# Kernel tuning notes

Measured on AMD Instinct MI355X. Metric: run time of the kernel, lower is better.

The kernel has to match this reference:

```python
import jax, jax.numpy as jnp
import numpy as np

D = 4096       # hidden_size
H = 32         # n_heads (tp_size=1)
DN = 128       # qk_nope_head_dim
DR = 64        # qk_rope_head_dim
DV = 128       # v_head_dim
QL = 1536      # q_lora_rank
KL = 512       # kv_lora_rank
S = 2048       # seqlen, start_pos = 0
EPS = 1e-6
SCALE = (DN + DR) ** -0.5  # softmax_scale (no yarn mscale: seqlen <= original_seq_len)
THETA = 10000.0


def _freqs(seqlen, dim, base=THETA):
    # precompute_freqs_cis without yarn correction (seqlen <= original_seq_len)
    inv = 1.0 / (base ** (np.arange(0, dim, 2, dtype=np.float32) / dim))
    f = np.outer(np.arange(seqlen, dtype=np.float32), inv)  # [S, dim//2]
    return jnp.asarray(np.cos(f)), jnp.asarray(np.sin(f))


def _rmsnorm(x, w):
    return x * jax.lax.rsqrt(jnp.mean(x * x, axis=-1, keepdims=True) + EPS) * w


def _rope(x, cos, sin):
    # x: [S, H, R]; complex rotation on consecutive pairs (view_as_complex semantics)
    S_, H_, R_ = x.shape
    xr = x.reshape(S_, H_, R_ // 2, 2)
    x0, x1 = xr[..., 0], xr[..., 1]
    c = cos[:, None, :]
    s = sin[:, None, :]
    y0 = x0 * c - x1 * s
    y1 = x0 * s + x1 * c
    return jnp.stack([y0, y1], axis=-1).reshape(S_, H_, R_)


def setup_inputs() -> dict:
    key = jax.random.key(0)
    ks = jax.random.split(key, 6)
    std = 0.02
    return {
        "x": jax.random.normal(ks[0], (S, D), jnp.float32),
        "wq_a": jax.random.normal(ks[1], (QL, D), jnp.float32) * std,
        "q_norm_w": jnp.ones((QL,), jnp.float32),
        "wq_b": jax.random.normal(ks[2], (H * (DN + DR), QL), jnp.float32) * std,
        "wkv_a": jax.random.normal(ks[3], (KL + DR, D), jnp.float32) * std,
        "kv_norm_w": jnp.ones((KL,), jnp.float32),
        "wkv_b": jax.random.normal(ks[4], (H * (DN + DV), KL), jnp.float32) * std,
        "wo": jax.random.normal(ks[5], (D, H * DV), jnp.float32) * std,
    }


def reference(x, wq_a, q_norm_w, wq_b, wkv_a, kv_norm_w, wkv_b, wo):
    cos, sin = _freqs(S, DR)

    # q path: low-rank down-proj + RMSNorm + up-proj
    q = _rmsnorm(x @ wq_a.T, q_norm_w) @ wq_b.T          # [S, H*(DN+DR)]
    q = q.reshape(S, H, DN + DR)
    q_nope, q_pe = q[..., :DN], q[..., DN:]
    q_pe = _rope(q_pe, cos, sin)                          # [S, H, DR]

    # kv path: joint latent + rope part
    kv_all = x @ wkv_a.T                                  # [S, KL+DR]
    kv = _rmsnorm(kv_all[:, :KL], kv_norm_w)              # latent kv cache [S, KL]
    k_pe = _rope(kv_all[:, None, KL:], cos, sin)[:, 0, :]  # pe cache [S, DR]

    # absorb k-up-projection into q (einsum 'shd,hdc->shc')
    wkv_b_r = wkv_b.reshape(H, DN + DV, KL)
    q_lat = jnp.einsum("shd,hdc->shc", q_nope, wkv_b_r[:, :DN])  # [S, H, KL]

    scores = (jnp.einsum("shc,tc->sht", q_lat, kv)
              + jnp.einsum("shr,tr->sht", q_pe, k_pe)) * SCALE   # [S, H, T]

    causal = jnp.arange(S)[:, None] >= jnp.arange(S)[None, :]     # [S, T]
    scores = jnp.where(causal[:, None, :], scores, -jnp.inf)
    p = jax.nn.softmax(scores, axis=-1)

    o_lat = jnp.einsum("sht,tc->shc", p, kv)                      # [S, H, KL]
    o = jnp.einsum("shc,hdc->shd", o_lat, wkv_b_r[:, DN:])        # [S, H, DV]
    return o.reshape(S, H * DV) @ wo.T                            # [S, D]
```

## Files before the change

kernel.cpp:

```cpp
#include <hip/hip_runtime.h>
#include <hip/hip_bf16.h>
#include <type_traits>

using bf16 = __hip_bfloat16;
typedef short v8s __attribute__((ext_vector_type(8)));
typedef float v4f __attribute__((ext_vector_type(4)));

#define DEV __device__ __forceinline__

constexpr float SCALE_ = 0.07216878364870322f;

DEV unsigned short bfu(float f) {
  bf16 h = __float2bfloat16(f);
  return __builtin_bit_cast(unsigned short, h);
}
DEV float b2f(short u) {
  unsigned int x = ((unsigned int)(unsigned short)u) << 16;
  return __builtin_bit_cast(float, x);
}

DEV void g2lds16(const void* g, void* l) {
  __builtin_amdgcn_global_load_lds(
      (const __attribute__((address_space(1))) unsigned int*)g,
      (__attribute__((address_space(3))) unsigned int*)l, 16, 0, 0);
}


__global__ void cast_kernel(const float* __restrict__ in, bf16* __restrict__ out, int n4) {
  int i = blockIdx.x * 256 + threadIdx.x;
  int stride = gridDim.x * 256;
  for (; i < n4; i += stride) {
    float4 v = ((const float4*)in)[i];
    ushort4 u;
    u.x = bfu(v.x); u.y = bfu(v.y); u.z = bfu(v.z); u.w = bfu(v.w);
    ((ushort4*)out)[i] = u;
  }
}

__global__ void cast_pad_kernel(const float* __restrict__ in, bf16* __restrict__ out) {
  int i = blockIdx.x * 256 + threadIdx.x;
  float4 v = make_float4(0.f, 0.f, 0.f, 0.f);
  if (i < 589824) v = ((const float4*)in)[i];
  ushort4 u;
  u.x = bfu(v.x); u.y = bfu(v.y); u.z = bfu(v.z); u.w = bfu(v.w);
  ((ushort4*)out)[i] = u;
}

__global__ void wkvbt_kernel(const float* __restrict__ wkvb, bf16* __restrict__ out) {
  int gid = blockIdx.x * 256 + threadIdx.x;
  int c8 = (gid & 63) * 8;
  int d8 = ((gid >> 6) & 15) * 8;
  int h = gid >> 10;
  float4 a[8][2];
#pragma unroll
  for (int r = 0; r < 8; ++r) {
    const float* p = wkvb + ((long)(h * 256 + d8 + r)) * 512 + c8;
    a[r][0] = *(const float4*)p;
    a[r][1] = *(const float4*)(p + 4);
  }
#pragma unroll
  for (int cc = 0; cc < 8; ++cc) {
    v8s o;
#pragma unroll
    for (int r = 0; r < 8; ++r) {
      float f = (cc < 4) ? ((const float*)&a[r][0])[cc] : ((const float*)&a[r][1])[cc - 4];
      o[r] = (short)bfu(f);
    }
    *(v8s*)(out + (long)h * 65536 + (c8 + cc) * 128 + d8) = o;
  }
}

__global__ void wkvbv_kernel(const float* __restrict__ wkvb, bf16* __restrict__ out) {
  int i = blockIdx.x * 256 + threadIdx.x;
  int c4 = i & 127, d = (i >> 7) & 127, h = i >> 14;
  float4 v = *(const float4*)(wkvb + ((long)(h * 256 + 128 + d)) * 512 + c4 * 4);
  ushort4 u;
  u.x = bfu(v.x); u.y = bfu(v.y); u.z = bfu(v.z); u.w = bfu(v.w);
  *(ushort4*)(out + ((long)(h * 128 + d)) * 512 + c4 * 4) = u;
}

__global__ void freqs_kernel(float* __restrict__ cosb, float* __restrict__ sinb) {
  int t = blockIdx.x * 256 + threadIdx.x;
  int s = t >> 5, i = t & 31;
  float inv = powf(10000.0f, -(float)(2 * i) / 64.0f);
  float f = (float)s * inv;
  cosb[t] = cosf(f);
  sinb[t] = sinf(f);
}

__global__ void rmsnorm_bf_kernel(const bf16* __restrict__ in, const float* __restrict__ w,
                                  bf16* __restrict__ out, int L, int ldin, int ldout) {
  int row = blockIdx.x;
  const bf16* x = in + (long)row * ldin;
  int L8 = L >> 3;
  float ss = 0.f;
  for (int i = threadIdx.x; i < L8; i += 256) {
    v8s v = *(const v8s*)(x + i * 8);
#pragma unroll
    for (int j = 0; j < 8; ++j) { float f = b2f(v[j]); ss += f * f; }
  }
#pragma unroll
  for (int d = 1; d < 64; d <<= 1) ss += __shfl_xor(ss, d);
  __shared__ float red[4];
  if ((threadIdx.x & 63) == 0) red[threadIdx.x >> 6] = ss;
  __syncthreads();
  float r = rsqrtf((red[0] + red[1] + red[2] + red[3]) / (float)L + 1e-6f);
  bf16* o = out + (long)row * ldout;
  for (int i = threadIdx.x; i < L8; i += 256) {
    v8s v = *(const v8s*)(x + i * 8);
    v8s u;
#pragma unroll
    for (int j = 0; j < 8; ++j)
      u[j] = (short)bfu(b2f(v[j]) * r * w[i * 8 + j]);
    *(v8s*)(o + i * 8) = u;
  }
}

__global__ void rope_kpe_kernel(const bf16* __restrict__ kvall, const float* __restrict__ cosb,
                                const float* __restrict__ sinb, bf16* __restrict__ keff) {
  int t = blockIdx.x * 256 + threadIdx.x;
  int s = t >> 5, i = t & 31;
  const bf16* p = kvall + (long)s * 640 + 512;
  float x0 = __bfloat162float(p[2 * i]), x1 = __bfloat162float(p[2 * i + 1]);
  float c = cosb[t], sn = sinb[t];
  bf16* o = keff + (long)s * 576 + 512;
  o[2 * i] = __float2bfloat16(x0 * c - x1 * sn);
  o[2 * i + 1] = __float2bfloat16(x0 * sn + x1 * c);
}

__global__ void rope_q_kernel(const bf16* __restrict__ qf, const float* __restrict__ cosb,
                              const float* __restrict__ sinb, bf16* __restrict__ qeff) {
  int t = blockIdx.x * 256 + threadIdx.x;
  int i = t & 31, h = (t >> 5) & 31, s = t >> 10;
  const bf16* p = qf + (long)s * 6144 + h * 192 + 128;
  float x0 = __bfloat162float(p[2 * i]), x1 = __bfloat162float(p[2 * i + 1]);
  float c = cosb[s * 32 + i], sn = sinb[s * 32 + i];
  bf16* o = qeff + (long)s * 18432 + h * 576 + 512;
  o[2 * i] = __float2bfloat16(x0 * c - x1 * sn);
  o[2 * i + 1] = __float2bfloat16(x0 * sn + x1 * c);
}

__global__ void vtrans_kernel(const bf16* __restrict__ keff, bf16* __restrict__ vT) {
  int gid = blockIdx.x * 256 + threadIdx.x;
  int t8 = (gid & 255) * 8, c8 = (gid >> 8) * 8;
  v8s in[8];
#pragma unroll
  for (int r = 0; r < 8; ++r)
    in[r] = *(const v8s*)(keff + (long)(t8 + r) * 576 + c8);
#pragma unroll
  for (int cc = 0; cc < 8; ++cc) {
    v8s o;
#pragma unroll
    for (int r = 0; r < 8; ++r) o[r] = in[r][cc];
    *(v8s*)(vT + (long)(c8 + cc) * 2048 + t8) = o;
  }
}

template <typename OutT>
__global__ __launch_bounds__(256, 3) void gemm_bt(
    const bf16* __restrict__ A, const bf16* __restrict__ B, OutT* __restrict__ C,
    int K, int lda, int ldb, int ldc, long sA, long sB, long sC) {
  __shared__ bf16 lA[4096];
  __shared__ bf16 lB[4096];
  const int tid = threadIdx.x;
  const int lane = tid & 63;
  const int w = tid >> 6, wm = w >> 1, wn = w & 1;
  const int r16 = lane & 15, kg = (lane >> 4) << 3;
  const int arow = tid >> 2, acol = (tid & 3) << 3;
  const bf16* Ab = A + (long)blockIdx.z * sA + (long)blockIdx.y * 128 * lda;
  const bf16* Bb = B + (long)blockIdx.z * sB + (long)blockIdx.x * 128 * ldb;
  v4f acc[4][4] = {};
  for (int k0 = 0; k0 < K; k0 += 32) {
    __syncthreads();
#pragma unroll
    for (int i = 0; i < 2; ++i) {
      g2lds16(Ab + (long)(i * 64 + arow) * lda + (k0 + acol), &lA[i * 2048 + w * 512]);
      g2lds16(Bb + (long)(i * 64 + arow) * ldb + (k0 + acol), &lB[i * 2048 + w * 512]);
    }
    __syncthreads();
    v8s af[4], bfr[4];
#pragma unroll
    for (int mi = 0; mi < 4; ++mi)
      af[mi] = *(const v8s*)&lA[(wm * 64 + mi * 16 + r16) * 32 + kg];
#pragma unroll
    for (int ni = 0; ni < 4; ++ni)
      bfr[ni] = *(const v8s*)&lB[(wn * 64 + ni * 16 + r16) * 32 + kg];
    __builtin_amdgcn_s_setprio(1);
#pragma unroll
    for (int mi = 0; mi < 4; ++mi)
#pragma unroll
      for (int ni = 0; ni < 4; ++ni)
        acc[mi][ni] = __builtin_amdgcn_mfma_f32_16x16x32_bf16(af[mi], bfr[ni], acc[mi][ni], 0, 0, 0);
    __builtin_amdgcn_s_setprio(0);
  }
  OutT* Cb = C + (long)blockIdx.z * sC + (long)(blockIdx.y * 128) * ldc + blockIdx.x * 128;
  const int cr = (lane >> 4) << 2;
#pragma unroll
  for (int mi = 0; mi < 4; ++mi)
#pragma unroll
    for (int ni = 0; ni < 4; ++ni)
#pragma unroll
      for (int j = 0; j < 4; ++j) {
        long idx = (long)(wm * 64 + mi * 16 + cr + j) * ldc + wn * 64 + ni * 16 + r16;
        float v = acc[mi][ni][j];
        if constexpr (std::is_same<OutT, float>::value) Cb[idx] = v;
        else Cb[idx] = __float2bfloat16(v);
      }
}

__global__ __launch_bounds__(512, 2) void attn_kernel(
    const bf16* __restrict__ qeff, const bf16* __restrict__ keff,
    const bf16* __restrict__ vT, bf16* __restrict__ olat) {
  __shared__ __align__(16) bf16 kl[32 * 576];
  __shared__ __align__(16) bf16 vl[512 * 32];
  const int tid = threadIdx.x, lane = tid & 63, w = tid >> 6;
  const int r16 = lane & 15, hi = lane >> 4;
  const int kg = hi << 3, cr = hi << 2;
  const int lb = blockIdx.y * 16 + blockIdx.x;
  const int p = lb & 255;
  const int g = p >> 5;
  const int h = p & 31;
  const int qt = (lb < 256) ? (15 - g) : g;
  const int qrow = qt * 128 + w * 16 + r16;
  const int rb = r16 & 7;

  const long qbase = (long)qrow * 18432 + h * 576;
  v8s qreg[18];
#pragma unroll
  for (int kk = 0; kk < 18; ++kk)
    qreg[kk] = __builtin_nontemporal_load((const v8s*)(qeff + qbase + kk * 32 + kg));

  v4f acc[32] = {};
  float mrow = -1e30f, lrow = 0.f;

  auto stageK = [&](int t0) {
#pragma unroll
    for (int it = 0; it < 5; ++it) {
      int D = it * 512 + tid;
      if (D < 2304) {
        int row = D / 72;
        int gg = D - row * 72;
        int gs = gg ^ (row & 7);
        g2lds16(keff + (long)(t0 + row) * 576 + gs * 8,
                (char*)kl + (it * 512 + w * 64) * 16);
      }
    }
  };
  auto stageV = [&](int t0) {
#pragma unroll
    for (int it = 0; it < 4; ++it) {
      int D = it * 512 + tid;
      int row = D >> 2;
      int s = (D & 3) ^ ((row >> 1) & 3);
      g2lds16(vT + (long)row * 2048 + t0 + s * 8,
              (char*)vl + (it * 512 + w * 64) * 16);
    }
  };

  const int nch = 4 * qt + 4;
  stageK(0);
  __syncthreads();

  for (int kc = 0; kc < nch; ++kc) {
    const int t0 = kc * 32;
    stageV(t0);

    const char* kb = (const char*)kl;
    v4f sf0 = {}, sf1 = {};
    __builtin_amdgcn_s_setprio(1);
#pragma unroll
    for (int kk = 0; kk < 18; ++kk) {
      int so = ((kk * 4 + hi) ^ rb) << 4;
      v8s b0 = *(const v8s*)(kb + r16 * 1152 + so);
      v8s b1 = *(const v8s*)(kb + (16 + r16) * 1152 + so);
      sf0 = __builtin_amdgcn_mfma_f32_16x16x32_bf16(b0, qreg[kk], sf0, 0, 0, 0);
      sf1 = __builtin_amdgcn_mfma_f32_16x16x32_bf16(b1, qreg[kk], sf1, 0, 0, 0);
    }
    __builtin_amdgcn_s_setprio(0);
    float s0[4], s1[4];
#pragma unroll
    for (int j = 0; j < 4; ++j) { s0[j] = sf0[j] * SCALE_; s1[j] = sf1[j] * SCALE_; }
    if (kc >= 4 * qt) {
#pragma unroll
      for (int j = 0; j < 4; ++j) {
        if (t0 + cr + j > qrow) s0[j] = -1e30f;
        if (t0 + 16 + cr + j > qrow) s1[j] = -1e30f;
      }
    }
    float mx = fmaxf(fmaxf(fmaxf(s0[0], s0[1]), fmaxf(s0[2], s0[3])),
                     fmaxf(fmaxf(s1[0], s1[1]), fmaxf(s1[2], s1[3])));
    mx = fmaxf(mx, __shfl_xor(mx, 16));
    mx = fmaxf(mx, __shfl_xor(mx, 32));
    if (!__all(mx <= mrow + 8.0f)) {
      float mn = fmaxf(mrow, mx);
      float alpha = __expf(mrow - mn);
      mrow = mn;
      lrow *= alpha;
      float af0 = __shfl(alpha, cr + 0), af1 = __shfl(alpha, cr + 1);
      float af2 = __shfl(alpha, cr + 2), af3 = __shfl(alpha, cr + 3);
#pragma unroll
      for (int c = 0; c < 32; ++c) {
        acc[c][0] *= af0; acc[c][1] *= af1; acc[c][2] *= af2; acc[c][3] *= af3;
      }
    }
    float p0[4], p1[4];
#pragma unroll
    for (int j = 0; j < 4; ++j) {
      p0[j] = __expf(s0[j] - mrow);
      p1[j] = __expf(s1[j] - mrow);
    }
    float rs = (p0[0] + p0[1]) + (p0[2] + p0[3]) + (p1[0] + p1[1]) + (p1[2] + p1[3]);
    rs += __shfl_xor(rs, 16);
    rs += __shfl_xor(rs, 32);
    lrow += rs;
    int u0 = (int)((unsigned)bfu(p0[0]) | ((unsigned)bfu(p0[1]) << 16));
    int u1 = (int)((unsigned)bfu(p0[2]) | ((unsigned)bfu(p0[3]) << 16));
    int v0 = (int)((unsigned)bfu(p1[0]) | ((unsigned)bfu(p1[1]) << 16));
    int v1 = (int)((unsigned)bfu(p1[2]) | ((unsigned)bfu(p1[3]) << 16));
    const int L1 = r16 + 32 * (hi & 1);
    const int L2 = L1 + 16;
    const bool lo = hi < 2;
    int d0a = __shfl(u0, L1), d0b = __shfl(v0, L1);
    int d1a = __shfl(u1, L1), d1b = __shfl(v1, L1);
    int d2a = __shfl(u0, L2), d2b = __shfl(v0, L2);
    int d3a = __shfl(u1, L2), d3b = __shfl(v1, L2);
    int4 pw = make_int4(lo ? d0a : d0b, lo ? d1a : d1b, lo ? d2a : d2b, lo ? d3a : d3b);
    v8s ap = __builtin_bit_cast(v8s, pw);

    __syncthreads();
    if (kc + 1 < nch) stageK(t0 + 32);

    __builtin_amdgcn_s_setprio(1);
#pragma unroll
    for (int c = 0; c < 32; ++c) {
      const int vrow = c * 16 + r16;
      const int vsw = (hi ^ ((vrow >> 1) & 3)) << 4;
      v8s bv = *(const v8s*)((const char*)vl + vrow * 64 + vsw);
      acc[c] = __builtin_amdgcn_mfma_f32_16x16x32_bf16(ap, bv, acc[c], 0, 0, 0);
    }
    __builtin_amdgcn_s_setprio(0);
    __syncthreads();
  }
  float linv0 = 1.0f / __shfl(lrow, cr + 0);
  float linv1 = 1.0f / __shfl(lrow, cr + 1);
  float linv2 = 1.0f / __shfl(lrow, cr + 2);
  float linv3 = 1.0f / __shfl(lrow, cr + 3);
  const long ob = (long)(qt * 128 + w * 16 + cr) * 16384 + h * 512 + r16;
#pragma unroll
  for (int c = 0; c < 32; ++c) {
    olat[ob + 0 * 16384 + c * 16] = __float2bfloat16(acc[c][0] * linv0);
    olat[ob + 1 * 16384 + c * 16] = __float2bfloat16(acc[c][1] * linv1);
    olat[ob + 2 * 16384 + c * 16] = __float2bfloat16(acc[c][2] * linv2);
    olat[ob + 3 * 16384 + c * 16] = __float2bfloat16(acc[c][3] * linv3);
  }
}


extern "C" void kernel_launch(void* const* d_in, const int* in_sizes, int n_in,
                              void* d_out, int out_size, void* d_ws, size_t ws_size,
                              hipStream_t stream) {
  const float* x = (const float*)d_in[0];
  const float* wq_a = (const float*)d_in[1];
  const float* q_norm_w = (const float*)d_in[2];
  const float* wq_b = (const float*)d_in[3];
  const float* wkv_a = (const float*)d_in[4];
  const float* kv_norm_w = (const float*)d_in[5];
  const float* wkv_b = (const float*)d_in[6];
  const float* wo = (const float*)d_in[7];
  char* ws = (char*)d_ws;

  float* cosb  = (float*)(ws + 0);
  float* sinb  = (float*)(ws + 262144);
  bf16* qeffb  = (bf16*)(ws + 524288);
  bf16* olat   = (bf16*)(ws + 76021760);
  bf16* keff   = (bf16*)(ws + 143130624);
  bf16* vTb    = (bf16*)(ws + 145489920);
  bf16* xb     = (bf16*)(ws + 76021760);
  bf16* wqab   = (bf16*)(ws + 92798976);
  bf16* wkvabp = (bf16*)(ws + 105381888);
  bf16* qa     = (bf16*)(ws + 110624768);
  bf16* kvall  = (bf16*)(ws + 116916224);
  bf16* qan    = (bf16*)(ws + 125829120);
  bf16* wqbb   = (bf16*)(ws + 76021760);
  bf16* qf     = (bf16*)(ws + 94896128);
  bf16* wkvb1t = (bf16*)(ws + 76021760);
  bf16* wkvbv  = (bf16*)(ws + 524288);
  bf16* obuf   = (bf16*)(ws + 4718592);
  bf16* wob    = (bf16*)(ws + 21495808);

  cast_kernel<<<2048, 256, 0, stream>>>(x, xb, 2097152);
  cast_kernel<<<2048, 256, 0, stream>>>(wq_a, wqab, 1572864);
  cast_pad_kernel<<<2560, 256, 0, stream>>>(wkv_a, wkvabp);
  freqs_kernel<<<256, 256, 0, stream>>>(cosb, sinb);

  gemm_bt<bf16><<<dim3(12, 16, 1), 256, 0, stream>>>(xb, wqab, qa, 4096, 4096, 4096, 1536, 0, 0, 0);
  gemm_bt<bf16><<<dim3(5, 16, 1), 256, 0, stream>>>(xb, wkvabp, kvall, 4096, 4096, 4096, 640, 0, 0, 0);

  rmsnorm_bf_kernel<<<2048, 256, 0, stream>>>(qa, q_norm_w, qan, 1536, 1536, 1536);
  rmsnorm_bf_kernel<<<2048, 256, 0, stream>>>(kvall, kv_norm_w, keff, 512, 640, 576);
  rope_kpe_kernel<<<256, 256, 0, stream>>>(kvall, cosb, sinb, keff);
  vtrans_kernel<<<64, 256, 0, stream>>>(keff, vTb);

  cast_kernel<<<2048, 256, 0, stream>>>(wq_b, wqbb, 2359296);
  gemm_bt<bf16><<<dim3(48, 16, 1), 256, 0, stream>>>(qan, wqbb, qf, 1536, 1536, 1536, 6144, 0, 0, 0);

  rope_q_kernel<<<8192, 256, 0, stream>>>(qf, cosb, sinb, qeffb);
  wkvbt_kernel<<<128, 256, 0, stream>>>(wkv_b, wkvb1t);
  gemm_bt<bf16><<<dim3(4, 16, 32), 256, 0, stream>>>(qf, wkvb1t, qeffb,
      128, 6144, 128, 18432, 192L, 65536L, 576L);

  attn_kernel<<<dim3(16, 32), 512, 0, stream>>>(qeffb, keff, vTb, olat);

  wkvbv_kernel<<<2048, 256, 0, stream>>>(wkv_b, wkvbv);
  gemm_bt<bf16><<<dim3(1, 16, 32), 256, 0, stream>>>(olat, wkvbv, obuf,
      512, 16384, 512, 4096, 512L, 65536L, 128L);

  cast_kernel<<<2048, 256, 0, stream>>>(wo, wob, 4194304);
  gemm_bt<float><<<dim3(32, 16, 1), 256, 0, stream>>>(obuf, wob, (float*)d_out,
      4096, 4096, 4096, 4096, 0, 0, 0);
}
```

Baseline: 727.9 us.

## Split long causal attention tiles across two blocks and merge with combine kernel

The eight longest query tiles (qt 8..15) now have their KV range split in half across two blocks (split-KV / flash-decoding style). Each half writes unnormalized partial outputs and row max/sum stats, and a new combine kernel rescales and merges the halves. Work units go from 512 to 768 blocks with a more even length distribution, which aims to reduce tail imbalance on the GPU. In exchange it adds extra bf16 partial writes and reads, a second kernel launch, and slight precision loss from storing unnormalized partials in bf16.

Result: faster. 707.5 us (-2.8%).

```diff
diff --git a/kernel.cpp b/kernel.cpp
--- a/kernel.cpp
+++ b/kernel.cpp
@@ -208,19 +208,25 @@
       }
 }
 
+__device__ const signed char U_QT[24] = {15,15,7,14,14,13,13,6,12,12,11,11,5,10,10,9,9,4,8,8,3,2,1,0};
+__device__ const signed char U_HF[24] = {0,1,-1,0,1,0,1,-1,0,1,0,1,-1,0,1,0,1,-1,0,1,-1,-1,-1,-1};
+
 __global__ __launch_bounds__(512, 2) void attn_kernel(
     const bf16* __restrict__ qeff, const bf16* __restrict__ keff,
-    const bf16* __restrict__ vT, bf16* __restrict__ olat) {
+    const bf16* __restrict__ vT, bf16* __restrict__ olat,
+    bf16* __restrict__ P1, float* __restrict__ mlb) {
   __shared__ __align__(16) bf16 kl[32 * 576];
   __shared__ __align__(16) bf16 vl[512 * 32];
   const int tid = threadIdx.x, lane = tid & 63, w = tid >> 6;
   const int r16 = lane & 15, hi = lane >> 4;
   const int kg = hi << 3, cr = hi << 2;
-  const int lb = blockIdx.y * 16 + blockIdx.x;
-  const int p = lb & 255;
-  const int g = p >> 5;
-  const int h = p & 31;
-  const int qt = (lb < 256) ? (15 - g) : g;
+  const int h = blockIdx.x;
+  const int u = blockIdx.y;
+  const int qt = U_QT[u];
+  const int hf = U_HF[u];
+  const int nch = 4 * qt + 4;
+  const int kc0 = (hf == 1) ? (nch >> 1) : 0;
+  const int kc1 = (hf == 0) ? (nch >> 1) : nch;
   const int qrow = qt * 128 + w * 16 + r16;
   const int rb = r16 & 7;
 
@@ -257,11 +263,10 @@
     }
   };
 
-  const int nch = 4 * qt + 4;
-  stageK(0);
+  stageK(kc0 * 32);
   __syncthreads();
 
-  for (int kc = 0; kc < nch; ++kc) {
+  for (int kc = kc0; kc < kc1; ++kc) {
     const int t0 = kc * 32;
     stageV(t0);
 
@@ -328,7 +333,7 @@
     v8s ap = __builtin_bit_cast(v8s, pw);
 
     __syncthreads();
-    if (kc + 1 < nch) stageK(t0 + 32);
+    if (kc + 1 < kc1) stageK(t0 + 32);
 
     __builtin_amdgcn_s_setprio(1);
 #pragma unroll
@@ -341,18 +346,57 @@
     __builtin_amdgcn_s_setprio(0);
     __syncthreads();
   }
-  float linv0 = 1.0f / __shfl(lrow, cr + 0);
-  float linv1 = 1.0f / __shfl(lrow, cr + 1);
-  float linv2 = 1.0f / __shfl(lrow, cr + 2);
-  float linv3 = 1.0f / __shfl(lrow, cr + 3);
-  const long ob = (long)(qt * 128 + w * 16 + cr) * 16384 + h * 512 + r16;
-#pragma unroll
-  for (int c = 0; c < 32; ++c) {
-    olat[ob + 0 * 16384 + c * 16] = __float2bfloat16(acc[c][0] * linv0);
-    olat[ob + 1 * 16384 + c * 16] = __float2bfloat16(acc[c][1] * linv1);
-    olat[ob + 2 * 16384 + c * 16] = __float2bfloat16(acc[c][2] * linv2);
-    olat[ob + 3 * 16384 + c * 16] = __float2bfloat16(acc[c][3] * linv3);
-  }
+  if (hf < 0) {
+    float linv0 = 1.0f / __shfl(lrow, cr + 0);
+    float linv1 = 1.0f / __shfl(lrow, cr + 1);
+    float linv2 = 1.0f / __shfl(lrow, cr + 2);
+    float linv3 = 1.0f / __shfl(lrow, cr + 3);
+    const long ob = (long)(qt * 128 + w * 16 + cr) * 16384 + h * 512 + r16;
+#pragma unroll
+    for (int c = 0; c < 32; ++c) {
+      olat[ob + 0 * 16384 + c * 16] = __float2bfloat16(acc[c][0] * linv0);
+      olat[ob + 1 * 16384 + c * 16] = __float2bfloat16(acc[c][1] * linv1);
+      olat[ob + 2 * 16384 + c * 16] = __float2bfloat16(acc[c][2] * linv2);
+      olat[ob + 3 * 16384 + c * 16] = __float2bfloat16(acc[c][3] * linv3);
+    }
+  } else {
+    if (hi == 0) {
+      float* mr = mlb + (((qrow - 1024) << 5) + h) * 4 + hf * 2;
+      mr[0] = mrow;
+      mr[1] = lrow;
+    }
+    bf16* dst = (hf == 0) ? olat : P1;
+    const int rbase = (hf == 0) ? (qt * 128) : (qt * 128 - 1024);
+    const long ob = (long)(rbase + w * 16 + cr) * 16384 + h * 512 + r16;
+#pragma unroll
+    for (int c = 0; c < 32; ++c) {
+      dst[ob + 0 * 16384 + c * 16] = __float2bfloat16(acc[c][0]);
+      dst[ob + 1 * 16384 + c * 16] = __float2bfloat16(acc[c][1]);
+      dst[ob + 2 * 16384 + c * 16] = __float2bfloat16(acc[c][2]);
+      dst[ob + 3 * 16384 + c * 16] = __float2bfloat16(acc[c][3]);
+    }
+  }
+}
+
+__global__ void combine_kernel(bf16* __restrict__ olat, const bf16* __restrict__ P1,
+                               const float* __restrict__ mlb) {
+  int gid = blockIdx.x * 256 + threadIdx.x;
+  int cg = gid & 63, h = (gid >> 6) & 31, r = gid >> 11;
+  const float* m4 = mlb + ((r << 5) + h) * 4;
+  float mA = m4[0], lA = m4[1], mB = m4[2], lB = m4[3];
+  float m = fmaxf(mA, mB);
+  float sA = __expf(mA - m), sB = __expf(mB - m);
+  float inv = 1.0f / (sA * lA + sB * lB);
+  sA *= inv; sB *= inv;
+  long oa = (long)(1024 + r) * 16384 + h * 512 + cg * 8;
+  long ob = (long)r * 16384 + h * 512 + cg * 8;
+  v8s a = *(const v8s*)(olat + oa);
+  v8s b = *(const v8s*)(P1 + ob);
+  v8s o;
+#pragma unroll
+  for (int j = 0; j < 8; ++j)
+    o[j] = (short)bfu(b2f(a[j]) * sA + b2f(b[j]) * sB);
+  *(v8s*)(olat + oa) = o;
 }
 
 
@@ -375,6 +419,8 @@
   bf16* olat   = (bf16*)(ws + 76021760);
   bf16* keff   = (bf16*)(ws + 143130624);
   bf16* vTb    = (bf16*)(ws + 145489920);
+  bf16* P1b    = (bf16*)(ws + 147587072);
+  float* mlb   = (float*)(ws + 181141504);
   bf16* xb     = (bf16*)(ws + 76021760);
   bf16* wqab   = (bf16*)(ws + 92798976);
   bf16* wkvabp = (bf16*)(ws + 105381888);
@@ -409,7 +455,8 @@
   gemm_bt<bf16><<<dim3(4, 16, 32), 256, 0, stream>>>(qf, wkvb1t, qeffb,
       128, 6144, 128, 18432, 192L, 65536L, 576L);
 
-  attn_kernel<<<dim3(16, 32), 512, 0, stream>>>(qeffb, keff, vTb, olat);
+  attn_kernel<<<dim3(32, 24), 512, 0, stream>>>(qeffb, keff, vTb, olat, P1b, mlb);
+  combine_kernel<<<8192, 256, 0, stream>>>(olat, P1b, mlb);
 
   wkvbv_kernel<<<2048, 256, 0, stream>>>(wkv_b, wkvbv);
   gemm_bt<bf16><<<dim3(1, 16, 32), 256, 0, stream>>>(olat, wkvbv, obuf,
```
